# Kernel tuning notes

Measured on AMD Instinct MI355X. Metric: run time of the kernel, lower is better.

Reference implementation:

```python
import jax, jax.numpy as jnp
import numpy as np

LEVEL_SIZES = [6, 24, 96, 384, 1536, 6144]
NUM_LABELS = sum(LEVEL_SIZES)  # 8190
IN_FEATURES = 768
BATCH = 8192


def setup_inputs() -> dict:
    key = jax.random.key(0)
    ks = jax.random.split(key, 2 * len(LEVEL_SIZES) + 1)
    inp = {"x": jax.random.normal(ks[0], (BATCH, IN_FEATURES), dtype=jnp.float32)}
    layer_in = IN_FEATURES
    for i, out in enumerate(LEVEL_SIZES):
        scale = 1.0 / np.sqrt(layer_in)
        inp[f"W{i}"] = jax.random.uniform(ks[2 * i + 1], (out, layer_in), jnp.float32, -scale, scale)
        inp[f"b{i}"] = jax.random.uniform(ks[2 * i + 2], (out,), jnp.float32, -scale, scale)
        layer_in += out
    # labels_by_level: a permutation of global label ids, split by level sizes
    rng = np.random.default_rng(42)
    inp["labels"] = jnp.asarray(rng.permutation(NUM_LABELS), dtype=jnp.int64)
    return inp


def reference(x, W0, b0, W1, b1, W2, b2, W3, b3, W4, b4, W5, b5, labels):
    Ws = [W0, W1, W2, W3, W4, W5]
    bs = [b0, b1, b2, b3, b4, b5]
    logits = jnp.zeros((x.shape[0], NUM_LABELS), dtype=x.dtype)
    cur = x
    off = 0
    for W, b, sz in zip(Ws, bs, LEVEL_SIZES):
        y = cur @ W.T + b  # [B, sz]
        lab = labels[off:off + sz]  # static slice: global columns for this level
        logits = logits.at[:, lab].set(y)
        cur = jax.nn.relu(jnp.concatenate([cur, y], axis=1))
        off += sz
    return logits
```

## Files before the change

kernel.cpp:

```cpp
#include <hip/hip_runtime.h>
#include <hip/hip_bf16.h>

#define BATCH 8192
#define NUM_LABELS 8190
#define CURW 2944
#define YW   8192

typedef __attribute__((ext_vector_type(4))) float f32x4;
typedef __attribute__((ext_vector_type(8))) short bf16x8;

#define VMCNT(n) asm volatile("s_waitcnt vmcnt(" #n ")" ::: "memory")
#define BAR() do { asm volatile("" ::: "memory"); __builtin_amdgcn_s_barrier(); asm volatile("" ::: "memory"); } while (0)
#define LGKM0() do { asm volatile("s_waitcnt lgkmcnt(0)" ::: "memory"); __builtin_amdgcn_sched_barrier(0); } while (0)

__device__ __forceinline__ unsigned short f2bf(float f) {
  unsigned u = __builtin_bit_cast(unsigned, f);
  unsigned r = u + 0x7fffu + ((u >> 16) & 1u);
  return (unsigned short)(r >> 16);
}
__device__ __forceinline__ float bf2f(unsigned short b) {
  return __builtin_bit_cast(float, (unsigned)b << 16);
}
__device__ __forceinline__ void gload_lds16(const void* g, void* l) {
  __builtin_amdgcn_global_load_lds(
      (const __attribute__((address_space(1))) void*)g,
      (__attribute__((address_space(3))) void*)l,
      16, 0, 0);
}

__global__ void k_prep_x(const float* __restrict__ x,
                         unsigned short* __restrict__ xraw,
                         unsigned short* __restrict__ cur) {
  const int TX = BATCH * 768 / 4;
  int i = blockIdx.x * 256 + threadIdx.x;
  if (i < TX) {
    float4 v = ((const float4*)x)[i];
    int e = i * 4;
    int row = e / 768;
    int col = e - row * 768;
    ushort4 a, c;
    a.x = f2bf(v.x); a.y = f2bf(v.y); a.z = f2bf(v.z); a.w = f2bf(v.w);
    c.x = f2bf(fmaxf(v.x, 0.f)); c.y = f2bf(fmaxf(v.y, 0.f));
    c.z = f2bf(fmaxf(v.z, 0.f)); c.w = f2bf(fmaxf(v.w, 0.f));
    *(ushort4*)(xraw + e) = a;
    *(ushort4*)(cur + (size_t)row * CURW + col) = c;
    return;
  }
  int j = i - TX;
  const int PP = 130;
  if (j < BATCH * PP) {
    int row = j / PP, p = j - row * PP;
    int col = p < 58 ? 774 + p : (p < 98 ? 856 + (p - 58) : 992 + (p - 98));
    cur[(size_t)row * CURW + col] = 0;
  }
}

__device__ __forceinline__ int pad2real(int kp) {
  if (kp < 774)  return kp;
  if (kp < 832)  return -1;
  if (kp < 856)  return 774 + (kp - 832);
  if (kp < 896)  return -1;
  if (kp < 992)  return 798 + (kp - 896);
  if (kp < 1024) return -1;
  if (kp < 1408) return 894 + (kp - 1024);
  return 1278 + (kp - 1408);
}

template<int KPAD, int KREAL, int NREAL>
__device__ __forceinline__ void convW(int rel, const float* __restrict__ W,
                                      unsigned short* __restrict__ Wp) {
  int n = rel / KPAD, kp = rel - n * KPAD;
  int kr = pad2real(kp);
  float v = 0.f;
  if (n < NREAL && kr >= 0) v = W[(size_t)n * KREAL + kr];
  Wp[rel] = f2bf(v);
}

__global__ void k_convert_w_all(const float* __restrict__ W0, const float* __restrict__ W1,
                                const float* __restrict__ W2, const float* __restrict__ W3,
                                const float* __restrict__ W4, const float* __restrict__ W5,
                                const int* __restrict__ labels, int* __restrict__ inv,
                                unsigned short* __restrict__ wp) {
  int i = blockIdx.x * 256 + threadIdx.x;
  if (i < NUM_LABELS) inv[labels[i]] = i;
  if (i >= 20963328) return;
  if (i < 319488) {
    if (i < 98304)       convW<768, 768, 6>  (i,          W0, wp);
    else if (i < 204800) convW<832, 774, 24> (i - 98304,  W1, wp + 98304);
    else                 convW<896, 798, 96> (i - 204800, W2, wp + 204800);
  } else {
    if (i < 712704)       convW<1024, 894, 384>  (i - 319488,  W3, wp + 319488);
    else if (i < 2875392) convW<1408, 1278, 1536>(i - 712704,  W4, wp + 712704);
    else                  convW<2944, 2814, 6144>(i - 2875392, W5, wp + 2875392);
  }
}

__global__ __launch_bounds__(256, 2) void k_fused_small(
    const unsigned short* __restrict__ xraw,
    const unsigned short* __restrict__ w0p,
    const unsigned short* __restrict__ w1p,
    const unsigned short* __restrict__ w2p,
    const float* __restrict__ b0, const float* __restrict__ b1,
    const float* __restrict__ b2,
    unsigned short* __restrict__ ybuf,
    unsigned short* __restrict__ cur) {
  __shared__ __align__(16) unsigned short As[32 * 1000];
  const int tid = threadIdx.x;
  const int l = tid & 63, w = tid >> 6;
  const int l15 = l & 15, q8 = (l >> 4) * 8;
  const int row0 = blockIdx.x * 32;
  const int mi = w >> 1;
  const int nj0 = w & 1;

  {
    const int r = tid >> 3, c8 = tid & 7;
    const unsigned short* src = xraw + (size_t)(row0 + r) * 768 + c8 * 96;
    unsigned short* dst = As + r * 1000 + c8 * 96;
#pragma unroll
    for (int i = 0; i < 12; ++i)
      *(bf16x8*)(dst + i * 8) = *(const bf16x8*)(src + i * 8);
    unsigned short* dz = As + r * 1000 + 768 + c8 * 28;
    ushort4 z = {0, 0, 0, 0};
#pragma unroll
    for (int i = 0; i < 7; ++i) *(ushort4*)(dz + i * 4) = z;
  }
  __syncthreads();

  auto level = [&](int K, int ntiles, int Nr, const unsigned short* W, int ldw,
                   const float* bias, int ycol, int ccol) {
    for (int n = nj0; n < ntiles; n += 2) {
      f32x4 acc = {0.f, 0.f, 0.f, 0.f};
      const unsigned short* wrow = W + (size_t)(n * 16 + l15) * ldw + q8;
      const unsigned short* arow = As + (mi * 16 + l15) * 1000 + q8;
#pragma unroll 2
      for (int k0 = 0; k0 < K; k0 += 32) {
        bf16x8 af = *(const bf16x8*)(arow + k0);
        bf16x8 bf = *(const bf16x8*)(wrow + k0);
        acc = __builtin_amdgcn_mfma_f32_16x16x32_bf16(af, bf, acc, 0, 0, 0);
      }
      int col = n * 16 + l15;
      if (col < Nr) {
        float bv = bias[col];
#pragma unroll
        for (int j = 0; j < 4; ++j) {
          int rl = mi * 16 + (l >> 4) * 4 + j;
          float y = acc[j] + bv;
          ybuf[(size_t)(row0 + rl) * YW + ycol + col] = f2bf(y);
          As[rl * 1000 + ccol + col] = f2bf(fmaxf(y, 0.f));
        }
      }
    }
    __syncthreads();
  };

  level(768, 1, 6,  w0p, 768, b0, 0,  768);

  {
    const int r = tid >> 3, c8 = tid & 7;
    unsigned short* p = As + r * 1000 + c8 * 96;
#pragma unroll
    for (int i = 0; i < 12; ++i) {
      bf16x8 v = *(bf16x8*)(p + i * 8);
#pragma unroll
      for (int j = 0; j < 8; ++j)
        if (((unsigned short)v[j]) & 0x8000u) v[j] = 0;
      *(bf16x8*)(p + i * 8) = v;
    }
  }
  __syncthreads();

  level(832, 2, 24, w1p, 832, b1, 6,  832);
  level(896, 6, 96, w2p, 896, b2, 30, 896);

  {
    const int r = tid >> 3, c8 = tid & 7;
    const unsigned short* srcl = As + r * 1000 + 768 + c8 * 28;
    unsigned short* dstg = cur + (size_t)(row0 + r) * CURW + 768 + c8 * 28;
#pragma unroll
    for (int i = 0; i < 7; ++i)
      *(ushort4*)(dstg + i * 4) = *(const ushort4*)(srcl + i * 4);
  }
}

__global__ __launch_bounds__(256, 2) void k_gemm(
    const unsigned short* __restrict__ A, int lda,
    const unsigned short* __restrict__ B, int ldb,
    const float* __restrict__ bias,
    unsigned short* __restrict__ ybuf,
    unsigned short* __restrict__ curout,
    int K, int Nreal, int yoff, int curoff) {
  __shared__ unsigned short Asmem[128 * 64];
  __shared__ unsigned short Bsmem[128 * 64];
  const int tid = threadIdx.x;
  const int lane = tid & 63;
  const int wid = tid >> 6;
  const int wr = wid >> 1, wc = wid & 1;
  const int brow = blockIdx.x * 128;
  const int bcol = blockIdx.y * 128;

  f32x4 acc[4][4] = {};

  for (int k0 = 0; k0 < K; k0 += 64) {
#pragma unroll
    for (int p = 0; p < 4; ++p) {
      int ch = wid * 4 + p;
      int eo = ch * 512 + lane * 8;
      int r = eo >> 6;
      int col = eo & 63;
      gload_lds16(A + (size_t)(brow + r) * lda + k0 + col, Asmem + ch * 512);
      gload_lds16(B + (size_t)(bcol + r) * ldb + k0 + col, Bsmem + ch * 512);
    }
    __syncthreads();
#pragma unroll
    for (int kk = 0; kk < 2; ++kk) {
      bf16x8 af[4], bfr[4];
      int colk = kk * 32 + (lane >> 4) * 8;
#pragma unroll
      for (int m = 0; m < 4; ++m)
        af[m] = *(const bf16x8*)(Asmem + (wr * 64 + m * 16 + (lane & 15)) * 64 + colk);
#pragma unroll
      for (int n = 0; n < 4; ++n)
        bfr[n] = *(const bf16x8*)(Bsmem + (wc * 64 + n * 16 + (lane & 15)) * 64 + colk);
#pragma unroll
      for (int m = 0; m < 4; ++m)
#pragma unroll
        for (int n = 0; n < 4; ++n)
          acc[m][n] = __builtin_amdgcn_mfma_f32_16x16x32_bf16(af[m], bfr[n], acc[m][n], 0, 0, 0);
    }
    __syncthreads();
  }

#pragma unroll
  for (int n = 0; n < 4; ++n) {
    int col = bcol + wc * 64 + n * 16 + (lane & 15);
    if (col >= Nreal) continue;
    float bv = bias[col];
#pragma unroll
    for (int m = 0; m < 4; ++m) {
#pragma unroll
      for (int j = 0; j < 4; ++j) {
        int row = brow + wr * 64 + m * 16 + (lane >> 4) * 4 + j;
        float y = acc[m][n][j] + bv;
        ybuf[(size_t)row * YW + yoff + col] = f2bf(y);
        if (curout) curout[(size_t)row * CURW + curoff + col] = f2bf(fmaxf(y, 0.f));
      }
    }
  }
}

__global__ __launch_bounds__(512, 2) void k_gemm256(
    const unsigned short* __restrict__ A, int lda,
    const unsigned short* __restrict__ B, int ldb,
    const float* __restrict__ bias,
    unsigned short* __restrict__ ybuf,
    unsigned short* __restrict__ curout,
    int K, int yoff, int curoff) {
  __shared__ __align__(16) unsigned short lds[65536];
  const int tid = threadIdx.x;
  const int l = tid & 63;
  const int w = tid >> 6;
  const int wr = w >> 2;
  const int wc = w & 3;
  const int l15 = l & 15;
  const int q8 = (l >> 4) * 8;
  const int sx = (l & 7) << 3;
  const int swz = ((l & 7) ^ (l >> 3)) * 8;

  const int bid = blockIdx.x;
  const int im = (bid & 7) * 4 + ((bid >> 3) & 3);
  const int in = bid >> 5;
  const int brow = im * 256, bcol = in * 256;

  const unsigned short* gAr0 = A + (size_t)(brow + w * 8 + (l >> 3)) * lda + swz;
  const unsigned short* gAr1 = gAr0 + (size_t)64 * lda;
  const unsigned short* gAr2 = gAr0 + (size_t)128 * lda;
  const unsigned short* gAr3 = gAr0 + (size_t)192 * lda;
  const unsigned short* gBr0 = B + (size_t)(bcol + w * 8 + (l >> 3)) * ldb + swz;
  const unsigned short* gBr1 = gBr0 + (size_t)64 * ldb;
  const unsigned short* gBr2 = gBr0 + (size_t)128 * ldb;
  const unsigned short* gBr3 = gBr0 + (size_t)192 * ldb;

  unsigned short* const dA00 = lds + w * 512;
  unsigned short* const dA01 = lds + 8192 + w * 512;
  unsigned short* const dA10 = lds + 16384 + w * 512;
  unsigned short* const dA11 = lds + 24576 + w * 512;
  unsigned short* const dB00 = lds + 32768 + w * 512;
  unsigned short* const dB01 = lds + 40960 + w * 512;
  unsigned short* const dB10 = lds + 49152 + w * 512;
  unsigned short* const dB11 = lds + 57344 + w * 512;

  const int cOff0 = (q8) ^ sx;
  const int cOff1 = (32 + q8) ^ sx;
  const int brB = (wc & 1) * 64;
  const unsigned short* const aB00 = lds + wr * 8192 + l15 * 64 + cOff0;
  const unsigned short* const aB01 = lds + wr * 8192 + l15 * 64 + cOff1;
  const unsigned short* const aB10 = lds + 16384 + wr * 8192 + l15 * 64 + cOff0;
  const unsigned short* const aB11 = lds + 16384 + wr * 8192 + l15 * 64 + cOff1;
  const unsigned short* const bB00 = lds + 32768 + (wc >> 1) * 8192 + (brB + l15) * 64 + cOff0;
  const unsigned short* const bB01 = lds + 32768 + (wc >> 1) * 8192 + (brB + l15) * 64 + cOff1;
  const unsigned short* const bB10 = lds + 49152 + (wc >> 1) * 8192 + (brB + l15) * 64 + cOff0;
  const unsigned short* const bB11 = lds + 49152 + (wc >> 1) * 8192 + (brB + l15) * 64 + cOff1;

  f32x4 acc[8][4] = {};
  bf16x8 aF[2][4], bF[2][4];

  auto stage2 = [&](const unsigned short* glo, const unsigned short* ghi,
                    unsigned short* dst, int koff) {
    gload_lds16(glo + koff, dst);
    gload_lds16(ghi + koff, dst + 4096);
  };
  auto ldA = [&](const unsigned short* b0, const unsigned short* b1, int mhalf) {
#pragma unroll
    for (int m = 0; m < 4; ++m) {
      aF[0][m] = *(const bf16x8*)(b0 + (mhalf * 64 + m * 16) * 64);
      aF[1][m] = *(const bf16x8*)(b1 + (mhalf * 64 + m * 16) * 64);
    }
  };
  auto ldB2 = [&](const unsigned short* b0, const unsigned short* b1, int nbase) {
#pragma unroll
    for (int n = 0; n < 2; ++n) {
      bF[0][nbase + n] = *(const bf16x8*)(b0 + (nbase + n) * 16 * 64);
      bF[1][nbase + n] = *(const bf16x8*)(b1 + (nbase + n) * 16 * 64);
    }
  };
  auto MMA = [&](int mbase, int nbase) {
    __builtin_amdgcn_s_setprio(1);
#pragma unroll
    for (int kk = 0; kk < 2; ++kk)
#pragma unroll
      for (int m = 0; m < 4; ++m)
#pragma unroll
        for (int n = 0; n < 2; ++n)
          acc[mbase + m][nbase + n] = __builtin_amdgcn_mfma_f32_16x16x32_bf16(
              aF[kk][m], bF[kk][nbase + n], acc[mbase + m][nbase + n], 0, 0, 0);
    __builtin_amdgcn_s_setprio(0);
  };

  const int KT = K >> 6;
  const int NT2 = KT >> 1;

  stage2(gBr0, gBr1, dB00, 0);
  stage2(gBr2, gBr3, dB01, 0);
  stage2(gAr0, gAr1, dA00, 0);
  stage2(gAr2, gAr3, dA01, 0);
  stage2(gBr0, gBr1, dB10, 64);
  stage2(gBr2, gBr3, dB11, 64);
  stage2(gAr0, gAr1, dA10, 64);
  VMCNT(6);
  BAR();
  ldB2(bB00, bB01, 0);

  for (int it = 0; it < NT2; ++it) {
    const bool more = (it + 1 < NT2);
    ldA(aB00, aB01, 0); stage2(gAr2, gAr3, dA11, 64);
    BAR(); LGKM0(); MMA(0, 0); BAR();
    ldB2(bB00, bB01, 2);
    BAR(); LGKM0(); MMA(0, 2); BAR();
    ldA(aB00, aB01, 1);
    if (more) stage2(gBr0, gBr1, dB00, 128);
    BAR(); LGKM0(); MMA(4, 0); BAR();
    if (more) { stage2(gBr2, gBr3, dB01, 128); stage2(gAr0, gAr1, dA00, 128); VMCNT(6); }
    else      { VMCNT(0); }
    BAR(); LGKM0(); MMA(4, 2); ldB2(bB10, bB11, 0); BAR();
    ldA(aB10, aB11, 0);
    if (more) stage2(gAr2, gAr3, dA01, 128);
    BAR(); LGKM0(); MMA(0, 0); BAR();
    ldB2(bB10, bB11, 2);
    BAR(); LGKM0(); MMA(0, 2); BAR();
    ldA(aB10, aB11, 1);
    if (more) stage2(gBr0, gBr1, dB10, 192);
    BAR(); LGKM0(); MMA(4, 0); BAR();
    if (more) { stage2(gBr2, gBr3, dB11, 192); stage2(gAr0, gAr1, dA10, 192); VMCNT(6); }
    BAR(); LGKM0(); MMA(4, 2);
    if (more) ldB2(bB00, bB01, 0);
    BAR();
    gAr0 += 128; gAr1 += 128; gAr2 += 128; gAr3 += 128;
    gBr0 += 128; gBr1 += 128; gBr2 += 128; gBr3 += 128;
  }

  const int j4 = (l >> 4) * 4;
  float bv[4];
#pragma unroll
  for (int n = 0; n < 4; ++n) bv[n] = bias[bcol + wc * 64 + n * 16 + l15];
#pragma unroll
  for (int m = 0; m < 8; ++m) {
    int rowb = brow + wr * 128 + m * 16 + j4;
#pragma unroll
    for (int j = 0; j < 4; ++j) {
      size_t rbase = (size_t)(rowb + j);
#pragma unroll
      for (int n = 0; n < 4; ++n) {
        int col = bcol + wc * 64 + n * 16 + l15;
        float y = acc[m][n][j] + bv[n];
        ybuf[rbase * YW + yoff + col] = f2bf(y);
        if (curout) curout[rbase * CURW + curoff + col] = f2bf(fmaxf(y, 0.f));
      }
    }
  }
}

__global__ void k_gather(const unsigned short* __restrict__ ybuf,
                         const int* __restrict__ inv,
                         float* __restrict__ out) {
  const int half = NUM_LABELS / 2;
  const long total = (long)BATCH * half;
  for (long b0 = (long)blockIdx.x * 1024; b0 < total; b0 += (long)gridDim.x * 1024) {
    long i = b0 + threadIdx.x;
#pragma unroll
    for (int u = 0; u < 4; ++u, i += 256) {
      if (i < total) {
        int row = (int)(i / half);
        int c2 = (int)(i - (long)row * half) * 2;
        int2 iv = *(const int2*)(inv + c2);
        const unsigned short* yr = ybuf + (size_t)row * YW;
        float2 v;
        v.x = bf2f(yr[iv.x]);
        v.y = bf2f(yr[iv.y]);
        *(float2*)(out + (size_t)row * NUM_LABELS + c2) = v;
      }
    }
  }
}

extern "C" void kernel_launch(void* const* d_in, const int* in_sizes, int n_in,
                              void* d_out, int out_size, void* d_ws, size_t ws_size,
                              hipStream_t stream) {
  const float* x = (const float*)d_in[0];
  const float* W[6];
  const float* bias[6];
  for (int i = 0; i < 6; ++i) {
    W[i] = (const float*)d_in[1 + 2 * i];
    bias[i] = (const float*)d_in[2 + 2 * i];
  }
  const int* labels = (const int*)d_in[13];
  float* out = (float*)d_out;

  char* ws = (char*)d_ws;
  unsigned short* xraw = (unsigned short*)(ws);
  unsigned short* cur  = (unsigned short*)(ws + 12582912);
  unsigned short* wp   = (unsigned short*)(ws + 60817408);
  unsigned short* ybuf = (unsigned short*)(ws + 102744064);
  int* inv             = (int*)(ws + 236961792);

  static const int Kpad[6]   = {768, 832, 896, 1024, 1408, 2944};
  static const int Nreal[6]  = {6, 24, 96, 384, 1536, 6144};
  static const int Npad[6]   = {128, 128, 128, 384, 1536, 6144};
  static const size_t woff[6] = {0, 98304, 204800, 319488, 712704, 2875392};
  static const int yoff[6]   = {0, 6, 30, 126, 510, 2046};
  static const int curoff[6] = {768, 832, 896, 1024, 1408, 0};

  {
    int tot = BATCH * 768 / 4 + BATCH * 130;
    k_prep_x<<<(tot + 255) / 256, 256, 0, stream>>>(x, xraw, cur);
  }
  k_convert_w_all<<<(20963328 + 255) / 256, 256, 0, stream>>>(
      W[0], W[1], W[2], W[3], W[4], W[5], labels, inv, wp);

  k_fused_small<<<BATCH / 32, 256, 0, stream>>>(
      xraw, wp + woff[0], wp + woff[1], wp + woff[2],
      bias[0], bias[1], bias[2], ybuf, cur);

  {
    dim3 grid(BATCH / 128, Npad[3] / 128);
    k_gemm<<<grid, 256, 0, stream>>>(cur, CURW, wp + woff[3], Kpad[3], bias[3], ybuf,
                                     cur, Kpad[3], Nreal[3], yoff[3], curoff[3]);
  }
  for (int i = 4; i < 6; ++i) {
    int nwg = (BATCH / 256) * (Npad[i] / 256);
    k_gemm256<<<nwg, 512, 0, stream>>>(cur, CURW, wp + woff[i], Kpad[i], bias[i], ybuf,
                                       (i < 5) ? cur : (unsigned short*)nullptr,
                                       Kpad[i], yoff[i], curoff[i]);
  }

  k_gather<<<8192, 256, 0, stream>>>(ybuf, inv, out);
}
```

Measured before the change: 648.1 us.

## Interleave LDS fragment loads with MFMAs via lgkmcnt ladder; flatten gather kernel

```diff
diff --git a/kernel.cpp b/kernel.cpp
--- a/kernel.cpp
+++ b/kernel.cpp
@@ -11,7 +11,7 @@
 
 #define VMCNT(n) asm volatile("s_waitcnt vmcnt(" #n ")" ::: "memory")
 #define BAR() do { asm volatile("" ::: "memory"); __builtin_amdgcn_s_barrier(); asm volatile("" ::: "memory"); } while (0)
-#define LGKM0() do { asm volatile("s_waitcnt lgkmcnt(0)" ::: "memory"); __builtin_amdgcn_sched_barrier(0); } while (0)
+#define WAITK(n) do { asm volatile("s_waitcnt lgkmcnt(" #n ")" ::: "memory"); __builtin_amdgcn_sched_barrier(0); } while (0)
 
 __device__ __forceinline__ unsigned short f2bf(float f) {
   unsigned u = __builtin_bit_cast(unsigned, f);
@@ -309,21 +309,36 @@
     gload_lds16(glo + koff, dst);
     gload_lds16(ghi + koff, dst + 4096);
   };
-  auto ldA = [&](const unsigned short* b0, const unsigned short* b1, int mhalf) {
+  auto ldAh = [&](const unsigned short* lo, const unsigned short* hi, int half) {
 #pragma unroll
     for (int m = 0; m < 4; ++m) {
-      aF[0][m] = *(const bf16x8*)(b0 + (mhalf * 64 + m * 16) * 64);
-      aF[1][m] = *(const bf16x8*)(b1 + (mhalf * 64 + m * 16) * 64);
-    }
-  };
-  auto ldB2 = [&](const unsigned short* b0, const unsigned short* b1, int nbase) {
+      aF[0][m] = *(const bf16x8*)(lo + (half * 64 + m * 16) * 64);
+      aF[1][m] = *(const bf16x8*)(hi + (half * 64 + m * 16) * 64);
+    }
+  };
+  auto ldB01f = [&](const unsigned short* lo, const unsigned short* hi) {
 #pragma unroll
     for (int n = 0; n < 2; ++n) {
-      bF[0][nbase + n] = *(const bf16x8*)(b0 + (nbase + n) * 16 * 64);
-      bF[1][nbase + n] = *(const bf16x8*)(b1 + (nbase + n) * 16 * 64);
-    }
-  };
-  auto MMA = [&](int mbase, int nbase) {
+      bF[0][n] = *(const bf16x8*)(lo + n * 16 * 64);
+      bF[1][n] = *(const bf16x8*)(hi + n * 16 * 64);
+    }
+  };
+  auto ldB23f = [&](const unsigned short* lo, const unsigned short* hi) {
+#pragma unroll
+    for (int n = 2; n < 4; ++n) {
+      bF[0][n] = *(const bf16x8*)(lo + n * 16 * 64);
+      bF[1][n] = *(const bf16x8*)(hi + n * 16 * 64);
+    }
+  };
+  auto MM4 = [&](int m, int mbase, int nbase) {
+#pragma unroll
+    for (int kk = 0; kk < 2; ++kk)
+#pragma unroll
+      for (int n = 0; n < 2; ++n)
+        acc[mbase + m][nbase + n] = __builtin_amdgcn_mfma_f32_16x16x32_bf16(
+            aF[kk][m], bF[kk][nbase + n], acc[mbase + m][nbase + n], 0, 0, 0);
+  };
+  auto MMAblk = [&](int mbase, int nbase) {
     __builtin_amdgcn_s_setprio(1);
 #pragma unroll
     for (int kk = 0; kk < 2; ++kk)
@@ -335,6 +350,15 @@
               aF[kk][m], bF[kk][nbase + n], acc[mbase + m][nbase + n], 0, 0, 0);
     __builtin_amdgcn_s_setprio(0);
   };
+
+#define LADDER(mb, nb, w0, w1, w2, w3) do { \
+    __builtin_amdgcn_s_setprio(1); \
+    WAITK(w0); MM4(0, mb, nb); \
+    WAITK(w1); MM4(1, mb, nb); \
+    WAITK(w2); MM4(2, mb, nb); \
+    WAITK(w3); MM4(3, mb, nb); \
+    __builtin_amdgcn_s_setprio(0); \
+  } while (0)
 
   const int KT = K >> 6;
   const int NT2 = KT >> 1;
@@ -348,35 +372,47 @@
   stage2(gAr0, gAr1, dA10, 64);
   VMCNT(6);
   BAR();
-  ldB2(bB00, bB01, 0);
+  ldB01f(bB00, bB01);
 
   for (int it = 0; it < NT2; ++it) {
     const bool more = (it + 1 < NT2);
-    ldA(aB00, aB01, 0); stage2(gAr2, gAr3, dA11, 64);
-    BAR(); LGKM0(); MMA(0, 0); BAR();
-    ldB2(bB00, bB01, 2);
-    BAR(); LGKM0(); MMA(0, 2); BAR();
-    ldA(aB00, aB01, 1);
+    stage2(gAr2, gAr3, dA11, 64);
+    ldAh(aB00, aB01, 0);
+    ldB23f(bB00, bB01);
+    LADDER(0, 0, 10, 8, 6, 4);
+    BAR();
+    MMAblk(0, 2);
+    BAR();
     if (more) stage2(gBr0, gBr1, dB00, 128);
-    BAR(); LGKM0(); MMA(4, 0); BAR();
+    ldAh(aB00, aB01, 1);
+    LADDER(4, 0, 6, 4, 2, 0);
+    BAR();
     if (more) { stage2(gBr2, gBr3, dB01, 128); stage2(gAr0, gAr1, dA00, 128); VMCNT(6); }
     else      { VMCNT(0); }
-    BAR(); LGKM0(); MMA(4, 2); ldB2(bB10, bB11, 0); BAR();
-    ldA(aB10, aB11, 0);
+    BAR();
+    ldB01f(bB10, bB11);
+    MMAblk(4, 2);
+    BAR();
     if (more) stage2(gAr2, gAr3, dA01, 128);
-    BAR(); LGKM0(); MMA(0, 0); BAR();
-    ldB2(bB10, bB11, 2);
-    BAR(); LGKM0(); MMA(0, 2); BAR();
-    ldA(aB10, aB11, 1);
+    ldAh(aB10, aB11, 0);
+    ldB23f(bB10, bB11);
+    LADDER(0, 0, 10, 8, 6, 4);
+    BAR();
+    MMAblk(0, 2);
+    BAR();
     if (more) stage2(gBr0, gBr1, dB10, 192);
-    BAR(); LGKM0(); MMA(4, 0); BAR();
+    ldAh(aB10, aB11, 1);
+    LADDER(4, 0, 6, 4, 2, 0);
+    BAR();
     if (more) { stage2(gBr2, gBr3, dB11, 192); stage2(gAr0, gAr1, dA10, 192); VMCNT(6); }
-    BAR(); LGKM0(); MMA(4, 2);
-    if (more) ldB2(bB00, bB01, 0);
+    BAR();
+    if (more) ldB01f(bB00, bB01);
+    MMAblk(4, 2);
     BAR();
     gAr0 += 128; gAr1 += 128; gAr2 += 128; gAr3 += 128;
     gBr0 += 128; gBr1 += 128; gBr2 += 128; gBr3 += 128;
   }
+#undef LADDER
 
   const int j4 = (l >> 4) * 4;
   float bv[4];
@@ -403,23 +439,16 @@
                          const int* __restrict__ inv,
                          float* __restrict__ out) {
   const int half = NUM_LABELS / 2;
-  const long total = (long)BATCH * half;
-  for (long b0 = (long)blockIdx.x * 1024; b0 < total; b0 += (long)gridDim.x * 1024) {
-    long i = b0 + threadIdx.x;
-#pragma unroll
-    for (int u = 0; u < 4; ++u, i += 256) {
-      if (i < total) {
-        int row = (int)(i / half);
-        int c2 = (int)(i - (long)row * half) * 2;
-        int2 iv = *(const int2*)(inv + c2);
-        const unsigned short* yr = ybuf + (size_t)row * YW;
-        float2 v;
-        v.x = bf2f(yr[iv.x]);
-        v.y = bf2f(yr[iv.y]);
-        *(float2*)(out + (size_t)row * NUM_LABELS + c2) = v;
-      }
-    }
-  }
+  int i = blockIdx.x * 256 + threadIdx.x;
+  if (i >= BATCH * half) return;
+  int row = i / half;
+  int c2 = (i - row * half) * 2;
+  int2 iv = *(const int2*)(inv + c2);
+  const unsigned short* yr = ybuf + (size_t)row * YW;
+  float2 v;
+  v.x = bf2f(yr[iv.x]);
+  v.y = bf2f(yr[iv.y]);
+  *(float2*)(out + (size_t)row * NUM_LABELS + c2) = v;
 }
 
 extern "C" void kernel_launch(void* const* d_in, const int* in_sizes, int n_in,
@@ -472,5 +501,5 @@
                                        Kpad[i], yoff[i], curoff[i]);
   }
 
-  k_gather<<<8192, 256, 0, stream>>>(ybuf, inv, out);
-}
+  k_gather<<<(BATCH * (NUM_LABELS / 2) + 255) / 256, 256, 0, stream>>>(ybuf, inv, out);
+}
```

Measured after the change: 607.2 us. 6.3% less time.

## Replace 512-thread 256x256 GEMM with 4-wave 256x128 tile kernel, per-row gather

Applied to the files above, without the earlier changes.

```diff
diff --git a/kernel.cpp b/kernel.cpp
--- a/kernel.cpp
+++ b/kernel.cpp
@@ -11,7 +11,7 @@
 
 #define VMCNT(n) asm volatile("s_waitcnt vmcnt(" #n ")" ::: "memory")
 #define BAR() do { asm volatile("" ::: "memory"); __builtin_amdgcn_s_barrier(); asm volatile("" ::: "memory"); } while (0)
-#define LGKM0() do { asm volatile("s_waitcnt lgkmcnt(0)" ::: "memory"); __builtin_amdgcn_sched_barrier(0); } while (0)
+#define WAITK(n) do { asm volatile("s_waitcnt lgkmcnt(" #n ")" ::: "memory"); __builtin_amdgcn_sched_barrier(0); } while (0)
 
 __device__ __forceinline__ unsigned short f2bf(float f) {
   unsigned u = __builtin_bit_cast(unsigned, f);
@@ -248,134 +248,122 @@
   }
 }
 
-__global__ __launch_bounds__(512, 2) void k_gemm256(
+__global__ __launch_bounds__(256, 2) void k_gemm_w4(
     const unsigned short* __restrict__ A, int lda,
     const unsigned short* __restrict__ B, int ldb,
     const float* __restrict__ bias,
     unsigned short* __restrict__ ybuf,
     unsigned short* __restrict__ curout,
     int K, int yoff, int curoff) {
-  __shared__ __align__(16) unsigned short lds[65536];
+  __shared__ __align__(16) unsigned short lds[24576];
   const int tid = threadIdx.x;
   const int l = tid & 63;
   const int w = tid >> 6;
-  const int wr = w >> 2;
-  const int wc = w & 3;
+  const int wr = w >> 1;
+  const int wc = w & 1;
   const int l15 = l & 15;
-  const int q8 = (l >> 4) * 8;
-  const int sx = (l & 7) << 3;
-  const int swz = ((l & 7) ^ (l >> 3)) * 8;
 
   const int bid = blockIdx.x;
   const int im = (bid & 7) * 4 + ((bid >> 3) & 3);
   const int in = bid >> 5;
-  const int brow = im * 256, bcol = in * 256;
-
-  const unsigned short* gAr0 = A + (size_t)(brow + w * 8 + (l >> 3)) * lda + swz;
-  const unsigned short* gAr1 = gAr0 + (size_t)64 * lda;
-  const unsigned short* gAr2 = gAr0 + (size_t)128 * lda;
-  const unsigned short* gAr3 = gAr0 + (size_t)192 * lda;
-  const unsigned short* gBr0 = B + (size_t)(bcol + w * 8 + (l >> 3)) * ldb + swz;
-  const unsigned short* gBr1 = gBr0 + (size_t)64 * ldb;
-  const unsigned short* gBr2 = gBr0 + (size_t)128 * ldb;
-  const unsigned short* gBr3 = gBr0 + (size_t)192 * ldb;
-
-  unsigned short* const dA00 = lds + w * 512;
-  unsigned short* const dA01 = lds + 8192 + w * 512;
-  unsigned short* const dA10 = lds + 16384 + w * 512;
-  unsigned short* const dA11 = lds + 24576 + w * 512;
-  unsigned short* const dB00 = lds + 32768 + w * 512;
-  unsigned short* const dB01 = lds + 40960 + w * 512;
-  unsigned short* const dB10 = lds + 49152 + w * 512;
-  unsigned short* const dB11 = lds + 57344 + w * 512;
-
-  const int cOff0 = (q8) ^ sx;
-  const int cOff1 = (32 + q8) ^ sx;
-  const int brB = (wc & 1) * 64;
-  const unsigned short* const aB00 = lds + wr * 8192 + l15 * 64 + cOff0;
-  const unsigned short* const aB01 = lds + wr * 8192 + l15 * 64 + cOff1;
-  const unsigned short* const aB10 = lds + 16384 + wr * 8192 + l15 * 64 + cOff0;
-  const unsigned short* const aB11 = lds + 16384 + wr * 8192 + l15 * 64 + cOff1;
-  const unsigned short* const bB00 = lds + 32768 + (wc >> 1) * 8192 + (brB + l15) * 64 + cOff0;
-  const unsigned short* const bB01 = lds + 32768 + (wc >> 1) * 8192 + (brB + l15) * 64 + cOff1;
-  const unsigned short* const bB10 = lds + 49152 + (wc >> 1) * 8192 + (brB + l15) * 64 + cOff0;
-  const unsigned short* const bB11 = lds + 49152 + (wc >> 1) * 8192 + (brB + l15) * 64 + cOff1;
+  const int brow = im * 256, bcol = in * 128;
+
+  const int srow = w * 16 + (l >> 2);
+  const int sslot = ((l & 3) ^ ((l >> 3) & 3)) * 8;
+  const unsigned short* gA = A + (size_t)(brow + srow) * lda + sslot;
+  const unsigned short* gB = B + (size_t)(bcol + srow) * ldb + sslot;
+
+  unsigned short* const sA0 = lds + w * 512;
+  unsigned short* const sA1 = lds + 8192 + w * 512;
+  unsigned short* const sB0 = lds + 16384 + w * 512;
+  unsigned short* const sB1 = lds + 20480 + w * 512;
+
+  const int rslot = ((l >> 4) ^ ((l >> 1) & 3)) * 8;
+  const unsigned short* const aR0 = lds + (wr * 128 + l15) * 32 + rslot;
+  const unsigned short* const aR1 = lds + 8192 + (wr * 128 + l15) * 32 + rslot;
+  const unsigned short* const bR0 = lds + 16384 + (wc * 64 + l15) * 32 + rslot;
+  const unsigned short* const bR1 = lds + 20480 + (wc * 64 + l15) * 32 + rslot;
 
   f32x4 acc[8][4] = {};
-  bf16x8 aF[2][4], bF[2][4];
-
-  auto stage2 = [&](const unsigned short* glo, const unsigned short* ghi,
-                    unsigned short* dst, int koff) {
-    gload_lds16(glo + koff, dst);
-    gload_lds16(ghi + koff, dst + 4096);
+  bf16x8 aF[8], bF[4];
+
+  auto stage0 = [&](int kt) {
+    const int ko = kt * 32;
+    gload_lds16(gA + ko, sA0);
+    gload_lds16(gA + (size_t)64 * lda + ko, sA0 + 2048);
+    gload_lds16(gA + (size_t)128 * lda + ko, sA0 + 4096);
+    gload_lds16(gA + (size_t)192 * lda + ko, sA0 + 6144);
+    gload_lds16(gB + ko, sB0);
+    gload_lds16(gB + (size_t)64 * ldb + ko, sB0 + 2048);
   };
-  auto ldA = [&](const unsigned short* b0, const unsigned short* b1, int mhalf) {
-#pragma unroll
-    for (int m = 0; m < 4; ++m) {
-      aF[0][m] = *(const bf16x8*)(b0 + (mhalf * 64 + m * 16) * 64);
-      aF[1][m] = *(const bf16x8*)(b1 + (mhalf * 64 + m * 16) * 64);
-    }
+  auto stage1 = [&](int kt) {
+    const int ko = kt * 32;
+    gload_lds16(gA + ko, sA1);
+    gload_lds16(gA + (size_t)64 * lda + ko, sA1 + 2048);
+    gload_lds16(gA + (size_t)128 * lda + ko, sA1 + 4096);
+    gload_lds16(gA + (size_t)192 * lda + ko, sA1 + 6144);
+    gload_lds16(gB + ko, sB1);
+    gload_lds16(gB + (size_t)64 * ldb + ko, sB1 + 2048);
   };
-  auto ldB2 = [&](const unsigned short* b0, const unsigned short* b1, int nbase) {
-#pragma unroll
-    for (int n = 0; n < 2; ++n) {
-      bF[0][nbase + n] = *(const bf16x8*)(b0 + (nbase + n) * 16 * 64);
-      bF[1][nbase + n] = *(const bf16x8*)(b1 + (nbase + n) * 16 * 64);
-    }
-  };
-  auto MMA = [&](int mbase, int nbase) {
+  auto body = [&](const unsigned short* aR, const unsigned short* bR) {
+    bF[0] = *(const bf16x8*)(bR);
+    bF[1] = *(const bf16x8*)(bR + 512);
+#pragma unroll
+    for (int m = 0; m < 8; ++m)
+      aF[m] = *(const bf16x8*)(aR + m * 512);
+    bF[2] = *(const bf16x8*)(bR + 1024);
+    bF[3] = *(const bf16x8*)(bR + 1536);
     __builtin_amdgcn_s_setprio(1);
-#pragma unroll
-    for (int kk = 0; kk < 2; ++kk)
-#pragma unroll
-      for (int m = 0; m < 4; ++m)
-#pragma unroll
-        for (int n = 0; n < 2; ++n)
-          acc[mbase + m][nbase + n] = __builtin_amdgcn_mfma_f32_16x16x32_bf16(
-              aF[kk][m], bF[kk][nbase + n], acc[mbase + m][nbase + n], 0, 0, 0);
+    WAITK(8);
+#pragma unroll
+    for (int m = 0; m < 2; ++m) {
+      acc[m][0] = __builtin_amdgcn_mfma_f32_16x16x32_bf16(aF[m], bF[0], acc[m][0], 0, 0, 0);
+      acc[m][1] = __builtin_amdgcn_mfma_f32_16x16x32_bf16(aF[m], bF[1], acc[m][1], 0, 0, 0);
+    }
+    WAITK(6);
+#pragma unroll
+    for (int m = 2; m < 4; ++m) {
+      acc[m][0] = __builtin_amdgcn_mfma_f32_16x16x32_bf16(aF[m], bF[0], acc[m][0], 0, 0, 0);
+      acc[m][1] = __builtin_amdgcn_mfma_f32_16x16x32_bf16(aF[m], bF[1], acc[m][1], 0, 0, 0);
+    }
+    WAITK(4);
+#pragma unroll
+    for (int m = 4; m < 6; ++m) {
+      acc[m][0] = __builtin_amdgcn_mfma_f32_16x16x32_bf16(aF[m], bF[0], acc[m][0], 0, 0, 0);
+      acc[m][1] = __builtin_amdgcn_mfma_f32_16x16x32_bf16(aF[m], bF[1], acc[m][1], 0, 0, 0);
+    }
+    WAITK(2);
+#pragma unroll
+    for (int m = 6; m < 8; ++m) {
+      acc[m][0] = __builtin_amdgcn_mfma_f32_16x16x32_bf16(aF[m], bF[0], acc[m][0], 0, 0, 0);
+      acc[m][1] = __builtin_amdgcn_mfma_f32_16x16x32_bf16(aF[m], bF[1], acc[m][1], 0, 0, 0);
+    }
+    WAITK(0);
+#pragma unroll
+    for (int m = 0; m < 8; ++m) {
+      acc[m][2] = __builtin_amdgcn_mfma_f32_16x16x32_bf16(aF[m], bF[2], acc[m][2], 0, 0, 0);
+      acc[m][3] = __builtin_amdgcn_mfma_f32_16x16x32_bf16(aF[m], bF[3], acc[m][3], 0, 0, 0);
+    }
     __builtin_amdgcn_s_setprio(0);
   };
 
-  const int KT = K >> 6;
+  const int KT = K >> 5;
   const int NT2 = KT >> 1;
 
-  stage2(gBr0, gBr1, dB00, 0);
-  stage2(gBr2, gBr3, dB01, 0);
-  stage2(gAr0, gAr1, dA00, 0);
-  stage2(gAr2, gAr3, dA01, 0);
-  stage2(gBr0, gBr1, dB10, 64);
-  stage2(gBr2, gBr3, dB11, 64);
-  stage2(gAr0, gAr1, dA10, 64);
-  VMCNT(6);
+  stage0(0);
+  VMCNT(0);
   BAR();
-  ldB2(bB00, bB01, 0);
-
-  for (int it = 0; it < NT2; ++it) {
-    const bool more = (it + 1 < NT2);
-    ldA(aB00, aB01, 0); stage2(gAr2, gAr3, dA11, 64);
-    BAR(); LGKM0(); MMA(0, 0); BAR();
-    ldB2(bB00, bB01, 2);
-    BAR(); LGKM0(); MMA(0, 2); BAR();
-    ldA(aB00, aB01, 1);
-    if (more) stage2(gBr0, gBr1, dB00, 128);
-    BAR(); LGKM0(); MMA(4, 0); BAR();
-    if (more) { stage2(gBr2, gBr3, dB01, 128); stage2(gAr0, gAr1, dA00, 128); VMCNT(6); }
-    else      { VMCNT(0); }
-    BAR(); LGKM0(); MMA(4, 2); ldB2(bB10, bB11, 0); BAR();
-    ldA(aB10, aB11, 0);
-    if (more) stage2(gAr2, gAr3, dA01, 128);
-    BAR(); LGKM0(); MMA(0, 0); BAR();
-    ldB2(bB10, bB11, 2);
-    BAR(); LGKM0(); MMA(0, 2); BAR();
-    ldA(aB10, aB11, 1);
-    if (more) stage2(gBr0, gBr1, dB10, 192);
-    BAR(); LGKM0(); MMA(4, 0); BAR();
-    if (more) { stage2(gBr2, gBr3, dB11, 192); stage2(gAr0, gAr1, dA10, 192); VMCNT(6); }
-    BAR(); LGKM0(); MMA(4, 2);
-    if (more) ldB2(bB00, bB01, 0);
+
+  for (int t = 0; t < NT2; ++t) {
+    const bool more = (t + 1 < NT2);
+    stage1(2 * t + 1);
+    body(aR0, bR0);
+    VMCNT(0);
     BAR();
-    gAr0 += 128; gAr1 += 128; gAr2 += 128; gAr3 += 128;
-    gBr0 += 128; gBr1 += 128; gBr2 += 128; gBr3 += 128;
+    if (more) stage0(2 * t + 2);
+    body(aR1, bR1);
+    if (more) VMCNT(0);
+    BAR();
   }
 
   const int j4 = (l >> 4) * 4;
@@ -399,25 +387,24 @@
   }
 }
 
-__global__ void k_gather(const unsigned short* __restrict__ ybuf,
-                         const int* __restrict__ inv,
-                         float* __restrict__ out) {
-  const int half = NUM_LABELS / 2;
-  const long total = (long)BATCH * half;
-  for (long b0 = (long)blockIdx.x * 1024; b0 < total; b0 += (long)gridDim.x * 1024) {
-    long i = b0 + threadIdx.x;
-#pragma unroll
-    for (int u = 0; u < 4; ++u, i += 256) {
-      if (i < total) {
-        int row = (int)(i / half);
-        int c2 = (int)(i - (long)row * half) * 2;
-        int2 iv = *(const int2*)(inv + c2);
-        const unsigned short* yr = ybuf + (size_t)row * YW;
-        float2 v;
-        v.x = bf2f(yr[iv.x]);
-        v.y = bf2f(yr[iv.y]);
-        *(float2*)(out + (size_t)row * NUM_LABELS + c2) = v;
-      }
+__global__ __launch_bounds__(256) void k_gather(
+    const unsigned short* __restrict__ ybuf,
+    const int* __restrict__ inv,
+    float* __restrict__ out) {
+  const int row = blockIdx.x;
+  const unsigned short* yr = ybuf + (size_t)row * YW;
+  float* orow = out + (size_t)row * NUM_LABELS;
+  const int t = threadIdx.x;
+#pragma unroll
+  for (int it = 0; it < 16; ++it) {
+    int idx = it * 256 + t;
+    if (idx < NUM_LABELS / 2) {
+      int c2 = idx * 2;
+      int2 iv = *(const int2*)(inv + c2);
+      float2 v;
+      v.x = bf2f(yr[iv.x]);
+      v.y = bf2f(yr[iv.y]);
+      *(float2*)(orow + c2) = v;
     }
   }
 }
@@ -465,12 +452,17 @@
     k_gemm<<<grid, 256, 0, stream>>>(cur, CURW, wp + woff[3], Kpad[3], bias[3], ybuf,
                                      cur, Kpad[3], Nreal[3], yoff[3], curoff[3]);
   }
-  for (int i = 4; i < 6; ++i) {
-    int nwg = (BATCH / 256) * (Npad[i] / 256);
-    k_gemm256<<<nwg, 512, 0, stream>>>(cur, CURW, wp + woff[i], Kpad[i], bias[i], ybuf,
-                                       (i < 5) ? cur : (unsigned short*)nullptr,
-                                       Kpad[i], yoff[i], curoff[i]);
-  }
-
-  k_gather<<<8192, 256, 0, stream>>>(ybuf, inv, out);
-}
+  {
+    int nwg = (BATCH / 256) * (Npad[4] / 128);
+    k_gemm_w4<<<nwg, 256, 0, stream>>>(cur, CURW, wp + woff[4], Kpad[4], bias[4], ybuf,
+                                       cur, Kpad[4], yoff[4], curoff[4]);
+  }
+  {
+    int nwg = (BATCH / 256) * (Npad[5] / 128);
+    k_gemm_w4<<<nwg, 256, 0, stream>>>(cur, CURW, wp + woff[5], Kpad[5], bias[5], ybuf,
+                                       (unsigned short*)nullptr,
+                                       Kpad[5], yoff[5], curoff[5]);
+  }
+
+  k_gather<<<BATCH, 256, 0, stream>>>(ybuf, inv, out);
+}
```

New measurement: 552.0 us. 14.8% less time.
